# Performance work log

Hardware: AMD Instinct MI355X
Metric: run time of the kernel (lower is better)

## Reference

```python
import jax, jax.numpy as jnp
import numpy as np

H, KVH, HD, HID = 16, 8, 128, 2048
GROUPS = H // KVH
THETA = 10000.0
EPS = 1e-6


def _rms_norm(x, w):
    # x: (..., HD), norm in fp32 like Qwen3RMSNorm
    xf = x.astype(jnp.float32)
    var = jnp.mean(xf * xf, axis=-1, keepdims=True)
    return (xf * jax.lax.rsqrt(var + EPS)).astype(x.dtype) * w


def _rope_cos_sin(position_ids, dtype):
    # position_ids: (B, S) int
    inv_freq = 1.0 / (THETA ** (jnp.arange(0, HD, 2, dtype=jnp.float32) / HD))  # (HD/2,)
    freqs = position_ids.astype(jnp.float32)[..., None] * inv_freq  # (B, S, HD/2)
    emb = jnp.concatenate([freqs, freqs], axis=-1)  # (B, S, HD)
    return jnp.cos(emb).astype(dtype), jnp.sin(emb).astype(dtype)


def _rotate_half(x):
    x1, x2 = jnp.split(x, 2, axis=-1)
    return jnp.concatenate([-x2, x1], axis=-1)


def _apply_rope(q, k, cos, sin):
    # q,k: (B, h, S, HD); cos,sin: (B, S, HD) -> broadcast over head dim
    cos = cos[:, None, :, :]
    sin = sin[:, None, :, :]
    q = q * cos + _rotate_half(q) * sin
    k = k * cos + _rotate_half(k) * sin
    return q, k


def setup_inputs() -> dict:
    key = jax.random.key(0)
    ks = jax.random.split(key, 10)
    B, S, L = 1, 2048, 2048
    w = 0.02
    return {
        "hidden_states": jax.random.normal(ks[0], (B, S, HID), jnp.float32),
        "context": jax.random.normal(ks[1], (B, L, HID), jnp.float32),
        "position_ids": jnp.arange(S, dtype=jnp.int64)[None, :].repeat(B, axis=0),
        "Wq": jax.random.normal(ks[2], (H * HD, HID), jnp.float32) * w,
        "Wk": jax.random.normal(ks[3], (KVH * HD, HID), jnp.float32) * w,
        "Wv": jax.random.normal(ks[4], (KVH * HD, HID), jnp.float32) * w,
        "Wo": jax.random.normal(ks[5], (HID, H * HD), jnp.float32) * w,
        "Wk_ctx": jax.random.normal(ks[6], (KVH * HD, HID), jnp.float32) * w,
        "Wv_ctx": jax.random.normal(ks[7], (KVH * HD, HID), jnp.float32) * w,
        "q_norm_w": jnp.ones((HD,), jnp.float32),
        "k_norm_w": jnp.ones((HD,), jnp.float32),
    }


def reference(hidden_states, context, position_ids, Wq, Wk, Wv, Wo, Wk_ctx, Wv_ctx, q_norm_w, k_norm_w):
    B, S, _ = hidden_states.shape
    L = context.shape[1]
    scaling = HD ** -0.5

    Q = (hidden_states @ Wq.T).reshape(B, S, H, HD).transpose(0, 2, 1, 3)    # (B,H,S,HD)
    K = (hidden_states @ Wk.T).reshape(B, S, KVH, HD).transpose(0, 2, 1, 3)  # (B,KVH,S,HD)
    V = (hidden_states @ Wv.T).reshape(B, S, KVH, HD).transpose(0, 2, 1, 3)

    Q = _rms_norm(Q, q_norm_w)
    K = _rms_norm(K, k_norm_w)

    cos, sin = _rope_cos_sin(position_ids, Q.dtype)
    Q, K = _apply_rope(Q, K, cos, sin)

    K_ctx = (context @ Wk_ctx.T).reshape(B, L, KVH, HD).transpose(0, 2, 1, 3)
    V_ctx = (context @ Wv_ctx.T).reshape(B, L, KVH, HD).transpose(0, 2, 1, 3)

    K_full = jnp.concatenate([K_ctx, K], axis=2)  # (B,KVH,L+S,HD)
    V_full = jnp.concatenate([V_ctx, V], axis=2)
    K_full = jnp.repeat(K_full, GROUPS, axis=1)   # (B,H,L+S,HD)
    V_full = jnp.repeat(V_full, GROUPS, axis=1)

    attn = jnp.einsum("bhsd,bhtd->bhst", Q, K_full) * scaling  # (B,H,S,L+S)
    attn = jax.nn.softmax(attn.astype(jnp.float32), axis=-1).astype(Q.dtype)
    out = jnp.einsum("bhst,bhtd->bhsd", attn, V_full)          # (B,H,S,HD)
    out = out.transpose(0, 2, 1, 3).reshape(B, S, H * HD)
    return out @ Wo.T
```

## Files before the change

kernel.cpp:

```cpp
#include <hip/hip_runtime.h>

typedef __bf16 bf16_t;
typedef __attribute__((ext_vector_type(8))) __bf16 bf16x8;
typedef __attribute__((ext_vector_type(4))) __bf16 bf16x4;
typedef __attribute__((ext_vector_type(4))) float f32x4;

#define LDA_PAD 72

__device__ __forceinline__ bf16x8 ld8(const float* g) {
  f32x4 a = *(const f32x4*)g;
  f32x4 b = *(const f32x4*)(g + 4);
  bf16x8 r;
  r[0] = (bf16_t)a[0]; r[1] = (bf16_t)a[1]; r[2] = (bf16_t)a[2]; r[3] = (bf16_t)a[3];
  r[4] = (bf16_t)b[0]; r[5] = (bf16_t)b[1]; r[6] = (bf16_t)b[2]; r[7] = (bf16_t)b[3];
  return r;
}
__device__ __forceinline__ bf16x8 ld8(const bf16_t* g) { return *(const bf16x8*)g; }

struct CvtArgs { const float* src[8]; bf16_t* dst[8]; };

__global__ __launch_bounds__(256) void cvt_all(CvtArgs a) {
  const int g = blockIdx.x * 256 + threadIdx.x;
  int seg, base;
  if (g < 1048576)      { if (g < 524288)  { seg = 0; base = 0; }
                          else             { seg = 1; base = 524288; } }
  else if (g < 2097152) { if (g < 1572864) { seg = 2; base = 1048576; }
                          else if (g < 1835008) { seg = 3; base = 1572864; }
                          else             { seg = 4; base = 1835008; } }
  else                  { if (g < 2359296) { seg = 5; base = 2097152; }
                          else if (g < 2621440) { seg = 6; base = 2359296; }
                          else             { seg = 7; base = 2621440; } }
  const size_t off = (size_t)(g - base) * 8;
  *(bf16x8*)(a.dst[seg] + off) = ld8(a.src[seg] + off);
}

template<typename TI>
__global__ __launch_bounds__(256) void proj_all(
    const TI* __restrict__ hs, const TI* __restrict__ ctx,
    const TI* __restrict__ Wq, const TI* __restrict__ Wk,
    const TI* __restrict__ Wv, const TI* __restrict__ Wkc,
    const TI* __restrict__ Wvc,
    bf16_t* __restrict__ Qb, bf16_t* __restrict__ Kb, bf16_t* __restrict__ Vt)
{
  __shared__ __align__(16) bf16_t lA[128 * LDA_PAD];
  __shared__ __align__(16) bf16_t lB[128 * LDA_PAD];
  const int tid = threadIdx.x, wave = tid >> 6, lane = tid & 63;
  const int quad = lane >> 4, lc = lane & 15;
  const int u = blockIdx.x;
  const int xcd = u & 7, v = u >> 3;
  const int op = v >> 5, w = v & 31;
  const int nh = w >> 4, mt0 = w & 15;
  const int n0 = (xcd + nh * 8) * 128, m0 = mt0 * 128;
  const TI* A; const TI* B;
  if (op == 0) { A = hs; B = Wq + (size_t)n0 * 2048; }
  else {
    A = (op == 1) ? ctx : hs;
    const TI* WK = (op == 1) ? Wkc : Wk;
    const TI* WV = (op == 1) ? Wvc : Wv;
    B = (n0 < 1024) ? WK + (size_t)n0 * 2048 : WV + (size_t)(n0 - 1024) * 2048;
  }
  const int mw = (wave >> 1) * 64, nw = (wave & 1) * 64;
  const int lr8 = lane >> 3, lc8 = (lane & 7) * 8;

  f32x4 acc[4][4];
#pragma unroll
  for (int i = 0; i < 4; ++i)
#pragma unroll
    for (int j = 0; j < 4; ++j) acc[i][j] = (f32x4){0.f, 0.f, 0.f, 0.f};

  bf16x8 pa[4], pb[4];
#pragma unroll
  for (int i = 0; i < 4; ++i) {
    const int row = (wave + 4 * i) * 8 + lr8;
    pa[i] = ld8(A + (size_t)(m0 + row) * 2048 + lc8);
    pb[i] = ld8(B + (size_t)row * 2048 + lc8);
  }

  for (int k0 = 0; k0 < 2048; k0 += 64) {
    __syncthreads();
#pragma unroll
    for (int i = 0; i < 4; ++i) {
      const int row = (wave + 4 * i) * 8 + lr8;
      *(bf16x8*)(lA + row * LDA_PAD + lc8) = pa[i];
      *(bf16x8*)(lB + row * LDA_PAD + lc8) = pb[i];
    }
    __syncthreads();
    if (k0 + 64 < 2048) {
      const int kn = k0 + 64;
#pragma unroll
      for (int i = 0; i < 4; ++i) {
        const int row = (wave + 4 * i) * 8 + lr8;
        pa[i] = ld8(A + (size_t)(m0 + row) * 2048 + kn + lc8);
        pb[i] = ld8(B + (size_t)row * 2048 + kn + lc8);
      }
    }
#pragma unroll
    for (int kk = 0; kk < 2; ++kk) {
      bf16x8 af[4], bfv[4];
#pragma unroll
      for (int mt = 0; mt < 4; ++mt)
        af[mt] = *(const bf16x8*)(lA + (mw + mt * 16 + lc) * LDA_PAD + kk * 32 + quad * 8);
#pragma unroll
      for (int nt = 0; nt < 4; ++nt)
        bfv[nt] = *(const bf16x8*)(lB + (nw + nt * 16 + lc) * LDA_PAD + kk * 32 + quad * 8);
#pragma unroll
      for (int mt = 0; mt < 4; ++mt)
#pragma unroll
        for (int nt = 0; nt < 4; ++nt)
          acc[mt][nt] = __builtin_amdgcn_mfma_f32_16x16x32_bf16(af[mt], bfv[nt], acc[mt][nt], 0, 0, 0);
    }
  }

  if (op == 0) {
#pragma unroll
    for (int mt = 0; mt < 4; ++mt)
#pragma unroll
      for (int nt = 0; nt < 4; ++nt)
#pragma unroll
        for (int r = 0; r < 4; ++r)
          Qb[(size_t)(m0 + mw + mt * 16 + quad * 4 + r) * 2048 + n0 + nw + nt * 16 + lc]
              = (bf16_t)acc[mt][nt][r];
  } else {
    const int t_off = (op == 1) ? 0 : 2048;
    if (n0 < 1024) {
#pragma unroll
      for (int mt = 0; mt < 4; ++mt)
#pragma unroll
        for (int nt = 0; nt < 4; ++nt)
#pragma unroll
          for (int r = 0; r < 4; ++r) {
            const int n = n0 + nw + nt * 16 + lc;
            const int kvh = n >> 7, dd = n & 127;
            const int t = t_off + m0 + mw + mt * 16 + quad * 4 + r;
            Kb[((size_t)kvh * 4096 + t) * 128 + dd] = (bf16_t)acc[mt][nt][r];
          }
    } else {
#pragma unroll
      for (int mt = 0; mt < 4; ++mt)
#pragma unroll
        for (int nt = 0; nt < 4; ++nt) {
          const int n = n0 - 1024 + nw + nt * 16 + lc;
          const int kvh = n >> 7, dd = n & 127;
          const int t = t_off + m0 + mw + mt * 16 + quad * 4;
          bf16x4 pk;
#pragma unroll
          for (int r = 0; r < 4; ++r) pk[r] = (bf16_t)acc[mt][nt][r];
          *(bf16x4*)(Vt + ((size_t)kvh * 128 + dd) * 4096 + t) = pk;
        }
    }
  }
}

__global__ __launch_bounds__(256) void normrope(
    bf16_t* __restrict__ Q, bf16_t* __restrict__ Kb,
    const float* __restrict__ qw, const float* __restrict__ kw)
{
  const int wave = threadIdx.x >> 6, lane = threadIdx.x & 63;
  const int row = blockIdx.x * 4 + wave;
  bf16_t* p; const float* w; int pos;
  if (row < 32768) {
    const int s = row >> 4, hh = row & 15;
    p = Q + (size_t)s * 2048 + hh * 128; w = qw; pos = s;
  } else {
    const int rk = row - 32768;
    const int s = rk >> 3, hh = rk & 7;
    p = Kb + ((size_t)hh * 4096 + 2048 + s) * 128; w = kw; pos = s;
  }
  const float x1 = (float)p[lane], x2 = (float)p[lane + 64];
  float ss = x1 * x1 + x2 * x2;
#pragma unroll
  for (int m = 1; m < 64; m <<= 1) ss += __shfl_xor(ss, m, 64);
  const float inv = rsqrtf(ss * (1.0f / 128.0f) + 1e-6f);
  const float y1 = x1 * inv * w[lane];
  const float y2 = x2 * inv * w[lane + 64];
  const float freq = (float)pos * exp2f((float)lane * (-13.287712379549449f / 64.0f));
  const float cb = cosf(freq), sb = sinf(freq);
  p[lane]      = (bf16_t)(y1 * cb - y2 * sb);
  p[lane + 64] = (bf16_t)(y2 * cb + y1 * sb);
}

template<int SPLIT>
__global__ __launch_bounds__(512, 4) void attn_kernel(
    const bf16_t* __restrict__ Q, const bf16_t* __restrict__ Kb,
    const bf16_t* __restrict__ Vt, bf16_t* __restrict__ O,
    float* __restrict__ Of, float* __restrict__ Lf)
{
  __shared__ __align__(16) char lK[64 * 256];
  __shared__ __align__(16) char lV[128 * 128];
  __shared__ __align__(16) char lP[8 * 2048];
  const int tid = threadIdx.x, wave = tid >> 6, lane = tid & 63;
  const int quad = lane >> 4, lc = lane & 15;
  const int bid = blockIdx.x;
  const int hk = bid & 7, qt = (bid >> 3) & 15, hsel = (bid >> 7) & 1;
  const int half = SPLIT ? (bid >> 8) : 0;
  const int h = hk * 2 + hsel;
  const int mrow0 = qt * 128 + wave * 16;
  const int tbase = half * 2048;
  const int tend = tbase + (SPLIT ? 2048 : 4096);
  const float cexp = 0.08838834764831845f * 1.4426950408889634f;

  bf16x8 qf[4];
  {
    const bf16_t* qb = Q + (size_t)(mrow0 + lc) * 2048 + h * 128 + quad * 8;
#pragma unroll
    for (int ks = 0; ks < 4; ++ks) qf[ks] = *(const bf16x8*)(qb + ks * 32);
  }
  float rs[4] = {0.f, 0.f, 0.f, 0.f};
  f32x4 oacc[8];
#pragma unroll
  for (int ot = 0; ot < 8; ++ot) oacc[ot] = (f32x4){0.f, 0.f, 0.f, 0.f};

  bf16x8 kp[2], vp[2];
  auto load_tile = [&](int t0) {
    const bf16_t* Kt = Kb + ((size_t)hk * 4096 + t0) * 128;
    const bf16_t* Vb = Vt + (size_t)hk * 524288 + t0;
#pragma unroll
    for (int i = 0; i < 2; ++i) {
      const int idx = wave * 2 + i;
      kp[i] = *(const bf16x8*)(Kt + (size_t)(idx * 4 + quad) * 128 + lc * 8);
      vp[i] = *(const bf16x8*)(Vb + (size_t)(idx * 8 + (lane >> 3)) * 4096 + (lane & 7) * 8);
    }
  };
  load_tile(tbase);

  char* lPw = lP + wave * 2048;
  const int sw_rd = (lc & 7) << 4;

  for (int t0 = tbase; t0 < tend; t0 += 64) {
    __syncthreads();
#pragma unroll
    for (int i = 0; i < 2; ++i) {
      const int idx = wave * 2 + i;
      const int kr = idx * 4 + quad;
      *(bf16x8*)(lK + kr * 256 + ((lc * 16) ^ ((kr & 7) << 4))) = kp[i];
      const int vr = idx * 8 + (lane >> 3);
      *(bf16x8*)(lV + vr * 128 + (((lane & 7) * 16) ^ ((vr & 7) << 4))) = vp[i];
    }
    __syncthreads();
    if (t0 + 64 < tend) load_tile(t0 + 64);

    f32x4 s[4];
#pragma unroll
    for (int nt = 0; nt < 4; ++nt) {
      f32x4 a = (f32x4){0.f, 0.f, 0.f, 0.f};
#pragma unroll
      for (int ks = 0; ks < 4; ++ks) {
        bf16x8 kf = *(const bf16x8*)(lK + (nt * 16 + lc) * 256 + ((ks * 64 + quad * 16) ^ sw_rd));
        a = __builtin_amdgcn_mfma_f32_16x16x32_bf16(qf[ks], kf, a, 0, 0, 0);
      }
      s[nt] = a;
    }

#pragma unroll
    for (int nt = 0; nt < 4; ++nt)
#pragma unroll
      for (int r = 0; r < 4; ++r) {
        const float pv = exp2f(s[nt][r] * cexp);
        rs[r] += pv;
        const int pr = quad * 4 + r;
        *(bf16_t*)(lPw + pr * 128 + ((nt * 32 + lc * 2) ^ ((pr & 7) << 4))) = (bf16_t)pv;
      }

#pragma unroll
    for (int ks2 = 0; ks2 < 2; ++ks2) {
      bf16x8 pf = *(const bf16x8*)(lPw + lc * 128 + ((ks2 * 64 + quad * 16) ^ sw_rd));
#pragma unroll
      for (int ot = 0; ot < 8; ++ot) {
        bf16x8 vf = *(const bf16x8*)(lV + (ot * 16 + lc) * 128 + ((ks2 * 64 + quad * 16) ^ sw_rd));
        oacc[ot] = __builtin_amdgcn_mfma_f32_16x16x32_bf16(pf, vf, oacc[ot], 0, 0, 0);
      }
    }
  }

  float l_r[4];
#pragma unroll
  for (int r = 0; r < 4; ++r) {
    float vv = rs[r];
    vv += __shfl_xor(vv, 1, 64);
    vv += __shfl_xor(vv, 2, 64);
    vv += __shfl_xor(vv, 4, 64);
    vv += __shfl_xor(vv, 8, 64);
    l_r[r] = vv;
  }
  if (SPLIT) {
    float* Oh = Of + (size_t)half * 4194304;
#pragma unroll
    for (int ot = 0; ot < 8; ++ot)
#pragma unroll
      for (int r = 0; r < 4; ++r)
        Oh[(size_t)(mrow0 + quad * 4 + r) * 2048 + h * 128 + ot * 16 + lc] = oacc[ot][r];
    if (lc == 0) {
      float* Lh = Lf + half * 32768 + h * 2048 + mrow0;
#pragma unroll
      for (int r = 0; r < 4; ++r) Lh[quad * 4 + r] = l_r[r];
    }
  } else {
#pragma unroll
    for (int ot = 0; ot < 8; ++ot)
#pragma unroll
      for (int r = 0; r < 4; ++r)
        O[(size_t)(mrow0 + quad * 4 + r) * 2048 + h * 128 + ot * 16 + lc]
            = (bf16_t)(oacc[ot][r] / l_r[r]);
  }
}

__global__ __launch_bounds__(256) void combine(
    const float* __restrict__ Of, const float* __restrict__ Lf,
    bf16_t* __restrict__ Ob)
{
  const int b = blockIdx.x;
  const int hk = b & 7, idx = b >> 3;
  const int h = hk * 2 + (idx & 1), sg = idx >> 1;
  const int t = threadIdx.x;
  const int s = sg * 16 + (t >> 4), d = (t & 15) * 8;
  const size_t e = (size_t)s * 2048 + h * 128 + d;
  const float l = Lf[h * 2048 + s] + Lf[32768 + h * 2048 + s];
  const float inv = 1.0f / l;
  f32x4 a0 = *(const f32x4*)(Of + e);
  f32x4 a1 = *(const f32x4*)(Of + e + 4);
  f32x4 b0 = *(const f32x4*)(Of + 4194304 + e);
  f32x4 b1 = *(const f32x4*)(Of + 4194304 + e + 4);
  bf16x8 rr;
#pragma unroll
  for (int j = 0; j < 4; ++j) {
    rr[j]     = (bf16_t)((a0[j] + b0[j]) * inv);
    rr[4 + j] = (bf16_t)((a1[j] + b1[j]) * inv);
  }
  *(bf16x8*)(Ob + e) = rr;
}

template<typename TB>
__global__ __launch_bounds__(256) void gemm_o(
    const bf16_t* __restrict__ A, const TB* __restrict__ Bw,
    float* __restrict__ C)
{
  __shared__ __align__(16) bf16_t lA[128 * LDA_PAD];
  __shared__ __align__(16) bf16_t lB[64 * LDA_PAD];
  const int tid = threadIdx.x, wave = tid >> 6, lane = tid & 63;
  const int quad = lane >> 4, lc = lane & 15;
  const int bid = blockIdx.x;
  const int xcd = bid & 7, v = bid >> 3;
  const int nh = v >> 4, mt0 = v & 15;
  const int n0 = (xcd + nh * 8) * 64, m0 = mt0 * 128;
  const int mw = (wave >> 1) * 64, nw = (wave & 1) * 32;
  const int lr8 = lane >> 3, lc8 = (lane & 7) * 8;

  f32x4 acc[4][2];
#pragma unroll
  for (int i = 0; i < 4; ++i)
#pragma unroll
    for (int j = 0; j < 2; ++j) acc[i][j] = (f32x4){0.f, 0.f, 0.f, 0.f};

  bf16x8 pa[4], pb[2];
#pragma unroll
  for (int i = 0; i < 4; ++i)
    pa[i] = ld8(A + (size_t)(m0 + (wave + 4 * i) * 8 + lr8) * 2048 + lc8);
#pragma unroll
  for (int i = 0; i < 2; ++i)
    pb[i] = ld8(Bw + (size_t)(n0 + i * 32 + wave * 8 + lr8) * 2048 + lc8);

  for (int k0 = 0; k0 < 2048; k0 += 64) {
    __syncthreads();
#pragma unroll
    for (int i = 0; i < 4; ++i)
      *(bf16x8*)(lA + ((wave + 4 * i) * 8 + lr8) * LDA_PAD + lc8) = pa[i];
#pragma unroll
    for (int i = 0; i < 2; ++i)
      *(bf16x8*)(lB + (i * 32 + wave * 8 + lr8) * LDA_PAD + lc8) = pb[i];
    __syncthreads();
    if (k0 + 64 < 2048) {
      const int kn = k0 + 64;
#pragma unroll
      for (int i = 0; i < 4; ++i)
        pa[i] = ld8(A + (size_t)(m0 + (wave + 4 * i) * 8 + lr8) * 2048 + kn + lc8);
#pragma unroll
      for (int i = 0; i < 2; ++i)
        pb[i] = ld8(Bw + (size_t)(n0 + i * 32 + wave * 8 + lr8) * 2048 + kn + lc8);
    }
#pragma unroll
    for (int kk = 0; kk < 2; ++kk) {
      bf16x8 af[4], bfv[2];
#pragma unroll
      for (int mt = 0; mt < 4; ++mt)
        af[mt] = *(const bf16x8*)(lA + (mw + mt * 16 + lc) * LDA_PAD + kk * 32 + quad * 8);
#pragma unroll
      for (int nt = 0; nt < 2; ++nt)
        bfv[nt] = *(const bf16x8*)(lB + (nw + nt * 16 + lc) * LDA_PAD + kk * 32 + quad * 8);
#pragma unroll
      for (int mt = 0; mt < 4; ++mt)
#pragma unroll
        for (int nt = 0; nt < 2; ++nt)
          acc[mt][nt] = __builtin_amdgcn_mfma_f32_16x16x32_bf16(af[mt], bfv[nt], acc[mt][nt], 0, 0, 0);
    }
  }
#pragma unroll
  for (int mt = 0; mt < 4; ++mt)
#pragma unroll
    for (int nt = 0; nt < 2; ++nt)
#pragma unroll
      for (int r = 0; r < 4; ++r)
        C[(size_t)(m0 + mw + mt * 16 + quad * 4 + r) * 2048 + n0 + nw + nt * 16 + lc]
            = acc[mt][nt][r];
}

extern "C" void kernel_launch(void* const* d_in, const int* in_sizes, int n_in,
                              void* d_out, int out_size, void* d_ws, size_t ws_size,
                              hipStream_t stream)
{
  const float* hs  = (const float*)d_in[0];
  const float* ctx = (const float*)d_in[1];
  const float* Wq  = (const float*)d_in[3];
  const float* Wk  = (const float*)d_in[4];
  const float* Wv  = (const float*)d_in[5];
  const float* Wo  = (const float*)d_in[6];
  const float* Wkc = (const float*)d_in[7];
  const float* Wvc = (const float*)d_in[8];
  const float* qw  = (const float*)d_in[9];
  const float* kw  = (const float*)d_in[10];

  bf16_t* Kb = (bf16_t*)d_out;
  bf16_t* Vt = Kb + (size_t)4 * 1024 * 1024;
  bf16_t* wsb = (bf16_t*)d_ws;
  const bool fast = ws_size >= (size_t)64 * 1024 * 1024;

  dim3 blk(256), ablk(512);
  if (fast) {
    bf16_t* hs_b  = wsb;
    bf16_t* ctx_b = wsb + (size_t)8  * 524288;
    bf16_t* Wq_b  = wsb + (size_t)16 * 524288;
    bf16_t* Wk_b  = wsb + (size_t)24 * 524288;
    bf16_t* Wv_b  = wsb + (size_t)28 * 524288;
    bf16_t* Wkc_b = wsb + (size_t)32 * 524288;
    bf16_t* Wvc_b = wsb + (size_t)36 * 524288;
    bf16_t* Wo_b  = wsb + (size_t)40 * 524288;
    bf16_t* Qb    = wsb + (size_t)48 * 524288;
    bf16_t* Ob    = wsb + (size_t)56 * 524288;
    float*  Of    = (float*)wsb;
    float*  Lfp   = (float*)(wsb + (size_t)16 * 1024 * 1024);
    CvtArgs ca;
    ca.src[0] = hs;  ca.dst[0] = hs_b;
    ca.src[1] = ctx; ca.dst[1] = ctx_b;
    ca.src[2] = Wq;  ca.dst[2] = Wq_b;
    ca.src[3] = Wk;  ca.dst[3] = Wk_b;
    ca.src[4] = Wv;  ca.dst[4] = Wv_b;
    ca.src[5] = Wkc; ca.dst[5] = Wkc_b;
    ca.src[6] = Wvc; ca.dst[6] = Wvc_b;
    ca.src[7] = Wo;  ca.dst[7] = Wo_b;
    cvt_all<<<dim3(12288), blk, 0, stream>>>(ca);
    proj_all<bf16_t><<<dim3(768), blk, 0, stream>>>(
        hs_b, ctx_b, Wq_b, Wk_b, Wv_b, Wkc_b, Wvc_b, Qb, Kb, Vt);
    normrope<<<dim3(12288), blk, 0, stream>>>(Qb, Kb, qw, kw);
    attn_kernel<1><<<dim3(512), ablk, 0, stream>>>(Qb, Kb, Vt, nullptr, Of, Lfp);
    combine<<<dim3(2048), blk, 0, stream>>>(Of, Lfp, Ob);
    gemm_o<bf16_t><<<dim3(512), blk, 0, stream>>>(Ob, Wo_b, (float*)d_out);
  } else {
    bf16_t* Qb = wsb;
    bf16_t* Ob = wsb + (size_t)8 * 524288;
    proj_all<float><<<dim3(768), blk, 0, stream>>>(
        hs, ctx, Wq, Wk, Wv, Wkc, Wvc, Qb, Kb, Vt);
    normrope<<<dim3(12288), blk, 0, stream>>>(Qb, Kb, qw, kw);
    attn_kernel<0><<<dim3(256), ablk, 0, stream>>>(Qb, Kb, Vt, Ob, nullptr, nullptr);
    gemm_o<float><<<dim3(512), blk, 0, stream>>>(Ob, Wo, (float*)d_out);
  }
}
```

Before: 350.2 us.

## Fuse RMSNorm and RoPE into projection GEMM epilogue, drop normrope kernel

Moves the per-head RMSNorm and rotary embedding for Q and the self K into the epilogue of the projection GEMM. Row sums of squares are reduced across the two column-waves through shared memory, and the rotate-half partner values are exchanged through a float staging buffer. This removes a separate kernel launch plus a full read and write of Q and K. In exchange it adds several block barriers and per-element cos/sin work inside the GEMM epilogue, which lengthens those blocks and could create load imbalance against the V and context-K blocks.

New measurement: 542.8 us. +55.0%, slower.

```diff
diff --git a/kernel.cpp b/kernel.cpp
--- a/kernel.cpp
+++ b/kernel.cpp
@@ -34,16 +34,18 @@
   *(bf16x8*)(a.dst[seg] + off) = ld8(a.src[seg] + off);
 }
 
-template<typename TI>
+template<typename TA>
 __global__ __launch_bounds__(256) void proj_all(
-    const TI* __restrict__ hs, const TI* __restrict__ ctx,
-    const TI* __restrict__ Wq, const TI* __restrict__ Wk,
-    const TI* __restrict__ Wv, const TI* __restrict__ Wkc,
-    const TI* __restrict__ Wvc,
+    const TA* __restrict__ hs, const TA* __restrict__ ctx,
+    const TA* __restrict__ Wq, const TA* __restrict__ Wk,
+    const TA* __restrict__ Wv, const TA* __restrict__ Wkc,
+    const TA* __restrict__ Wvc,
+    const float* __restrict__ qw, const float* __restrict__ kw,
     bf16_t* __restrict__ Qb, bf16_t* __restrict__ Kb, bf16_t* __restrict__ Vt)
 {
-  __shared__ __align__(16) bf16_t lA[128 * LDA_PAD];
-  __shared__ __align__(16) bf16_t lB[128 * LDA_PAD];
+  __shared__ __align__(16) char smem[2 * 128 * LDA_PAD * 2];
+  bf16_t* lA = (bf16_t*)smem;
+  bf16_t* lB = lA + 128 * LDA_PAD;
   const int tid = threadIdx.x, wave = tid >> 6, lane = tid & 63;
   const int quad = lane >> 4, lc = lane & 15;
   const int u = blockIdx.x;
@@ -51,12 +53,12 @@
   const int op = v >> 5, w = v & 31;
   const int nh = w >> 4, mt0 = w & 15;
   const int n0 = (xcd + nh * 8) * 128, m0 = mt0 * 128;
-  const TI* A; const TI* B;
+  const TA* A; const TA* B;
   if (op == 0) { A = hs; B = Wq + (size_t)n0 * 2048; }
   else {
     A = (op == 1) ? ctx : hs;
-    const TI* WK = (op == 1) ? Wkc : Wk;
-    const TI* WV = (op == 1) ? Wvc : Wv;
+    const TA* WK = (op == 1) ? Wkc : Wk;
+    const TA* WV = (op == 1) ? Wvc : Wv;
     B = (n0 < 1024) ? WK + (size_t)n0 * 2048 : WV + (size_t)(n0 - 1024) * 2048;
   }
   const int mw = (wave >> 1) * 64, nw = (wave & 1) * 64;
@@ -111,72 +113,113 @@
     }
   }
 
-  if (op == 0) {
+  const bool normQ = (op == 0);
+  const bool normK = (op == 2) && (n0 < 1024);
+  if (normQ || normK) {
+    const float* wgt = normQ ? qw : kw;
+    float wf[4];
+#pragma unroll
+    for (int nt = 0; nt < 4; ++nt) wf[nt] = wgt[nw + nt * 16 + lc];
+
+    float ss[4][4];
 #pragma unroll
     for (int mt = 0; mt < 4; ++mt)
 #pragma unroll
+      for (int r = 0; r < 4; ++r) {
+        float s = 0.f;
+#pragma unroll
+        for (int nt = 0; nt < 4; ++nt) s += acc[mt][nt][r] * acc[mt][nt][r];
+#pragma unroll
+        for (int m = 1; m < 16; m <<= 1) s += __shfl_xor(s, m, 16);
+        ss[mt][r] = s;
+      }
+    __syncthreads();
+    float* ssbuf = (float*)(smem + 32768);
+    if (lc == 0) {
+#pragma unroll
+      for (int mt = 0; mt < 4; ++mt)
+#pragma unroll
+        for (int r = 0; r < 4; ++r)
+          ssbuf[((wave >> 1) * 64 + mt * 16 + quad * 4 + r) * 2 + (wave & 1)] = ss[mt][r];
+    }
+    __syncthreads();
+    float inv[4][4];
+#pragma unroll
+    for (int mt = 0; mt < 4; ++mt)
+#pragma unroll
+      for (int r = 0; r < 4; ++r) {
+        const int row = (wave >> 1) * 64 + mt * 16 + quad * 4 + r;
+        const float t = ssbuf[row * 2] + ssbuf[row * 2 + 1];
+        inv[mt][r] = rsqrtf(t * (1.0f / 128.0f) + 1e-6f);
+      }
+
+    float invf[4];
+#pragma unroll
+    for (int nt = 0; nt < 4; ++nt)
+      invf[nt] = exp2f((float)(nt * 16 + lc) * (-13.287712379549449f / 64.0f));
+
+    float* ybuf = (float*)smem;
+    const int kvh = n0 >> 7;
+#pragma unroll
+    for (int mt = 0; mt < 4; ++mt) {
+      __syncthreads();
+#pragma unroll
       for (int nt = 0; nt < 4; ++nt)
 #pragma unroll
-        for (int r = 0; r < 4; ++r)
-          Qb[(size_t)(m0 + mw + mt * 16 + quad * 4 + r) * 2048 + n0 + nw + nt * 16 + lc]
-              = (bf16_t)acc[mt][nt][r];
+        for (int r = 0; r < 4; ++r) {
+          const int yrow = (wave >> 1) * 16 + quad * 4 + r;
+          ybuf[yrow * 132 + nw + nt * 16 + lc] = acc[mt][nt][r] * inv[mt][r] * wf[nt];
+        }
+      __syncthreads();
+#pragma unroll
+      for (int nt = 0; nt < 4; ++nt)
+#pragma unroll
+        for (int r = 0; r < 4; ++r) {
+          const int yrow = (wave >> 1) * 16 + quad * 4 + r;
+          const int col = nw + nt * 16 + lc;
+          const int row = (wave >> 1) * 64 + mt * 16 + quad * 4 + r;
+          const float yv = acc[mt][nt][r] * inv[mt][r] * wf[nt];
+          const float y2 = ybuf[yrow * 132 + (col ^ 64)];
+          const int pos = m0 + row;
+          const float fr = (float)pos * invf[nt];
+          const float cb = cosf(fr), sb = sinf(fr);
+          const float out = (nw == 0) ? (yv * cb - y2 * sb) : (yv * cb + y2 * sb);
+          if (normQ) {
+            Qb[(size_t)(m0 + row) * 2048 + n0 + col] = (bf16_t)out;
+          } else {
+            const int t = 2048 + m0 + row;
+            Kb[((size_t)kvh * 4096 + t) * 128 + col] = (bf16_t)out;
+          }
+        }
+    }
+  } else if (n0 < 1024) {
+    const int t_off = 0;
+#pragma unroll
+    for (int mt = 0; mt < 4; ++mt)
+#pragma unroll
+      for (int nt = 0; nt < 4; ++nt)
+#pragma unroll
+        for (int r = 0; r < 4; ++r) {
+          const int n = n0 + nw + nt * 16 + lc;
+          const int kvh = n >> 7, dd = n & 127;
+          const int t = t_off + m0 + mw + mt * 16 + quad * 4 + r;
+          Kb[((size_t)kvh * 4096 + t) * 128 + dd] = (bf16_t)acc[mt][nt][r];
+        }
   } else {
     const int t_off = (op == 1) ? 0 : 2048;
-    if (n0 < 1024) {
-#pragma unroll
-      for (int mt = 0; mt < 4; ++mt)
-#pragma unroll
-        for (int nt = 0; nt < 4; ++nt)
-#pragma unroll
-          for (int r = 0; r < 4; ++r) {
-            const int n = n0 + nw + nt * 16 + lc;
-            const int kvh = n >> 7, dd = n & 127;
-            const int t = t_off + m0 + mw + mt * 16 + quad * 4 + r;
-            Kb[((size_t)kvh * 4096 + t) * 128 + dd] = (bf16_t)acc[mt][nt][r];
-          }
-    } else {
-#pragma unroll
-      for (int mt = 0; mt < 4; ++mt)
-#pragma unroll
-        for (int nt = 0; nt < 4; ++nt) {
-          const int n = n0 - 1024 + nw + nt * 16 + lc;
-          const int kvh = n >> 7, dd = n & 127;
-          const int t = t_off + m0 + mw + mt * 16 + quad * 4;
-          bf16x4 pk;
-#pragma unroll
-          for (int r = 0; r < 4; ++r) pk[r] = (bf16_t)acc[mt][nt][r];
-          *(bf16x4*)(Vt + ((size_t)kvh * 128 + dd) * 4096 + t) = pk;
-        }
-    }
-  }
-}
-
-__global__ __launch_bounds__(256) void normrope(
-    bf16_t* __restrict__ Q, bf16_t* __restrict__ Kb,
-    const float* __restrict__ qw, const float* __restrict__ kw)
-{
-  const int wave = threadIdx.x >> 6, lane = threadIdx.x & 63;
-  const int row = blockIdx.x * 4 + wave;
-  bf16_t* p; const float* w; int pos;
-  if (row < 32768) {
-    const int s = row >> 4, hh = row & 15;
-    p = Q + (size_t)s * 2048 + hh * 128; w = qw; pos = s;
-  } else {
-    const int rk = row - 32768;
-    const int s = rk >> 3, hh = rk & 7;
-    p = Kb + ((size_t)hh * 4096 + 2048 + s) * 128; w = kw; pos = s;
-  }
-  const float x1 = (float)p[lane], x2 = (float)p[lane + 64];
-  float ss = x1 * x1 + x2 * x2;
-#pragma unroll
-  for (int m = 1; m < 64; m <<= 1) ss += __shfl_xor(ss, m, 64);
-  const float inv = rsqrtf(ss * (1.0f / 128.0f) + 1e-6f);
-  const float y1 = x1 * inv * w[lane];
-  const float y2 = x2 * inv * w[lane + 64];
-  const float freq = (float)pos * exp2f((float)lane * (-13.287712379549449f / 64.0f));
-  const float cb = cosf(freq), sb = sinf(freq);
-  p[lane]      = (bf16_t)(y1 * cb - y2 * sb);
-  p[lane + 64] = (bf16_t)(y2 * cb + y1 * sb);
+#pragma unroll
+    for (int mt = 0; mt < 4; ++mt)
+#pragma unroll
+      for (int nt = 0; nt < 4; ++nt) {
+        const int n = n0 - 1024 + nw + nt * 16 + lc;
+        const int kvh = n >> 7, dd = n & 127;
+        const int t = t_off + m0 + mw + mt * 16 + quad * 4;
+        bf16x4 pk;
+#pragma unroll
+        for (int r = 0; r < 4; ++r) pk[r] = (bf16_t)acc[mt][nt][r];
+        *(bf16x4*)(Vt + ((size_t)kvh * 128 + dd) * 4096 + t) = pk;
+      }
+  }
 }
 
 template<int SPLIT>
@@ -448,8 +491,7 @@
     ca.src[7] = Wo;  ca.dst[7] = Wo_b;
     cvt_all<<<dim3(12288), blk, 0, stream>>>(ca);
     proj_all<bf16_t><<<dim3(768), blk, 0, stream>>>(
-        hs_b, ctx_b, Wq_b, Wk_b, Wv_b, Wkc_b, Wvc_b, Qb, Kb, Vt);
-    normrope<<<dim3(12288), blk, 0, stream>>>(Qb, Kb, qw, kw);
+        hs_b, ctx_b, Wq_b, Wk_b, Wv_b, Wkc_b, Wvc_b, qw, kw, Qb, Kb, Vt);
     attn_kernel<1><<<dim3(512), ablk, 0, stream>>>(Qb, Kb, Vt, nullptr, Of, Lfp);
     combine<<<dim3(2048), blk, 0, stream>>>(Of, Lfp, Ob);
     gemm_o<bf16_t><<<dim3(512), blk, 0, stream>>>(Ob, Wo_b, (float*)d_out);
@@ -457,8 +499,7 @@
     bf16_t* Qb = wsb;
     bf16_t* Ob = wsb + (size_t)8 * 524288;
     proj_all<float><<<dim3(768), blk, 0, stream>>>(
-        hs, ctx, Wq, Wk, Wv, Wkc, Wvc, Qb, Kb, Vt);
-    normrope<<<dim3(12288), blk, 0, stream>>>(Qb, Kb, qw, kw);
+        hs, ctx, Wq, Wk, Wv, Wkc, Wvc, qw, kw, Qb, Kb, Vt);
     attn_kernel<0><<<dim3(256), ablk, 0, stream>>>(Qb, Kb, Vt, Ob, nullptr, nullptr);
     gemm_o<float><<<dim3(512), blk, 0, stream>>>(Ob, Wo, (float*)d_out);
   }
```

## Fuse QK norm+RoPE into projection epilogue and combine into attention via grid barrier

Applied to the files above, without the earlier changes.

Drops the separate normrope kernel: the projection GEMM now stages each 128x128 Q/K tile in shared memory and applies RMSNorm and RoPE before writing. It also drops the separate combine launch: after writing split partials, attention blocks sync through an atomic counter grid barrier and then merge the two halves themselves. This saves two launches and a round trip of Q/K through global memory. The cost is recomputing cos/sin per element and a spin-wait barrier that only works if all 512 blocks are resident at once.

New measurement: 530.6 us. +51.5%, slower.

```diff
diff --git a/kernel.cpp b/kernel.cpp
--- a/kernel.cpp
+++ b/kernel.cpp
@@ -40,13 +40,17 @@
     const TI* __restrict__ Wq, const TI* __restrict__ Wk,
     const TI* __restrict__ Wv, const TI* __restrict__ Wkc,
     const TI* __restrict__ Wvc,
-    bf16_t* __restrict__ Qb, bf16_t* __restrict__ Kb, bf16_t* __restrict__ Vt)
+    const float* __restrict__ qw, const float* __restrict__ kw,
+    bf16_t* __restrict__ Qb, bf16_t* __restrict__ Kb, bf16_t* __restrict__ Vt,
+    unsigned int* __restrict__ ctr)
 {
-  __shared__ __align__(16) bf16_t lA[128 * LDA_PAD];
-  __shared__ __align__(16) bf16_t lB[128 * LDA_PAD];
+  __shared__ __align__(16) char smem[2 * 128 * LDA_PAD * 2];
+  bf16_t* lA = (bf16_t*)smem;
+  bf16_t* lB = lA + 128 * LDA_PAD;
   const int tid = threadIdx.x, wave = tid >> 6, lane = tid & 63;
   const int quad = lane >> 4, lc = lane & 15;
   const int u = blockIdx.x;
+  if (ctr && u == 0 && tid == 0) *ctr = 0;
   const int xcd = u & 7, v = u >> 3;
   const int op = v >> 5, w = v & 31;
   const int nh = w >> 4, mt0 = w & 15;
@@ -111,79 +115,88 @@
     }
   }
 
-  if (op == 0) {
+  const bool normQ = (op == 0);
+  const bool normK = (op == 2) && (n0 < 1024);
+  if (normQ || normK) {
+    bf16_t* yb = (bf16_t*)smem;
+    __syncthreads();
 #pragma unroll
     for (int mt = 0; mt < 4; ++mt)
 #pragma unroll
       for (int nt = 0; nt < 4; ++nt)
 #pragma unroll
         for (int r = 0; r < 4; ++r)
-          Qb[(size_t)(m0 + mw + mt * 16 + quad * 4 + r) * 2048 + n0 + nw + nt * 16 + lc]
+          yb[(mw + mt * 16 + quad * 4 + r) * 136 + nw + nt * 16 + lc]
               = (bf16_t)acc[mt][nt][r];
+    __syncthreads();
+    const int rowi = tid >> 1, half = tid & 1;
+    const float* wgt = normQ ? qw : kw;
+    const bf16_t* rowp = yb + rowi * 136;
+    float ss = 0.f;
+#pragma unroll
+    for (int c = 0; c < 8; ++c) {
+      bf16x8 vv = *(const bf16x8*)(rowp + half * 64 + c * 8);
+#pragma unroll
+      for (int j = 0; j < 8; ++j) { const float f = (float)vv[j]; ss += f * f; }
+    }
+    ss += __shfl_xor(ss, 1, 64);
+    const float inv = rsqrtf(ss * (1.0f / 128.0f) + 1e-6f);
+    const int pos = m0 + rowi;
+    const int kvh = n0 >> 7;
+    bf16_t* dst = normQ ? (Qb + (size_t)pos * 2048 + n0 + half * 64)
+                        : (Kb + ((size_t)kvh * 4096 + 2048 + m0 + rowi) * 128 + half * 64);
+    const float sgn = half ? 1.f : -1.f;
+#pragma unroll
+    for (int c = 0; c < 8; ++c) {
+      bf16x8 vv = *(const bf16x8*)(rowp + half * 64 + c * 8);
+      bf16x8 v2 = *(const bf16x8*)(rowp + (half ^ 1) * 64 + c * 8);
+      bf16x8 o;
+#pragma unroll
+      for (int j = 0; j < 8; ++j) {
+        const int dd = half * 64 + c * 8 + j;
+        const int dm = c * 8 + j;
+        const float y  = (float)vv[j] * inv * wgt[dd];
+        const float y2 = (float)v2[j] * inv * wgt[dd ^ 64];
+        const float fr = (float)pos * exp2f((float)dm * (-13.287712379549449f / 64.0f));
+        o[j] = (bf16_t)(y * cosf(fr) + sgn * y2 * sinf(fr));
+      }
+      *(bf16x8*)dst = o; dst += 8;
+    }
+  } else if (n0 < 1024) {
+#pragma unroll
+    for (int mt = 0; mt < 4; ++mt)
+#pragma unroll
+      for (int nt = 0; nt < 4; ++nt)
+#pragma unroll
+        for (int r = 0; r < 4; ++r) {
+          const int n = n0 + nw + nt * 16 + lc;
+          const int kvh = n >> 7, dd = n & 127;
+          const int t = m0 + mw + mt * 16 + quad * 4 + r;
+          Kb[((size_t)kvh * 4096 + t) * 128 + dd] = (bf16_t)acc[mt][nt][r];
+        }
   } else {
     const int t_off = (op == 1) ? 0 : 2048;
-    if (n0 < 1024) {
-#pragma unroll
-      for (int mt = 0; mt < 4; ++mt)
-#pragma unroll
-        for (int nt = 0; nt < 4; ++nt)
-#pragma unroll
-          for (int r = 0; r < 4; ++r) {
-            const int n = n0 + nw + nt * 16 + lc;
-            const int kvh = n >> 7, dd = n & 127;
-            const int t = t_off + m0 + mw + mt * 16 + quad * 4 + r;
-            Kb[((size_t)kvh * 4096 + t) * 128 + dd] = (bf16_t)acc[mt][nt][r];
-          }
-    } else {
-#pragma unroll
-      for (int mt = 0; mt < 4; ++mt)
-#pragma unroll
-        for (int nt = 0; nt < 4; ++nt) {
-          const int n = n0 - 1024 + nw + nt * 16 + lc;
-          const int kvh = n >> 7, dd = n & 127;
-          const int t = t_off + m0 + mw + mt * 16 + quad * 4;
-          bf16x4 pk;
-#pragma unroll
-          for (int r = 0; r < 4; ++r) pk[r] = (bf16_t)acc[mt][nt][r];
-          *(bf16x4*)(Vt + ((size_t)kvh * 128 + dd) * 4096 + t) = pk;
-        }
-    }
-  }
-}
-
-__global__ __launch_bounds__(256) void normrope(
-    bf16_t* __restrict__ Q, bf16_t* __restrict__ Kb,
-    const float* __restrict__ qw, const float* __restrict__ kw)
-{
-  const int wave = threadIdx.x >> 6, lane = threadIdx.x & 63;
-  const int row = blockIdx.x * 4 + wave;
-  bf16_t* p; const float* w; int pos;
-  if (row < 32768) {
-    const int s = row >> 4, hh = row & 15;
-    p = Q + (size_t)s * 2048 + hh * 128; w = qw; pos = s;
-  } else {
-    const int rk = row - 32768;
-    const int s = rk >> 3, hh = rk & 7;
-    p = Kb + ((size_t)hh * 4096 + 2048 + s) * 128; w = kw; pos = s;
-  }
-  const float x1 = (float)p[lane], x2 = (float)p[lane + 64];
-  float ss = x1 * x1 + x2 * x2;
-#pragma unroll
-  for (int m = 1; m < 64; m <<= 1) ss += __shfl_xor(ss, m, 64);
-  const float inv = rsqrtf(ss * (1.0f / 128.0f) + 1e-6f);
-  const float y1 = x1 * inv * w[lane];
-  const float y2 = x2 * inv * w[lane + 64];
-  const float freq = (float)pos * exp2f((float)lane * (-13.287712379549449f / 64.0f));
-  const float cb = cosf(freq), sb = sinf(freq);
-  p[lane]      = (bf16_t)(y1 * cb - y2 * sb);
-  p[lane + 64] = (bf16_t)(y2 * cb + y1 * sb);
+#pragma unroll
+    for (int mt = 0; mt < 4; ++mt)
+#pragma unroll
+      for (int nt = 0; nt < 4; ++nt) {
+        const int n = n0 - 1024 + nw + nt * 16 + lc;
+        const int kvh = n >> 7, dd = n & 127;
+        const int t = t_off + m0 + mw + mt * 16 + quad * 4;
+        bf16x4 pk;
+#pragma unroll
+        for (int r = 0; r < 4; ++r) pk[r] = (bf16_t)acc[mt][nt][r];
+        *(bf16x4*)(Vt + ((size_t)kvh * 128 + dd) * 4096 + t) = pk;
+      }
+  }
 }
 
 template<int SPLIT>
 __global__ __launch_bounds__(512, 4) void attn_kernel(
     const bf16_t* __restrict__ Q, const bf16_t* __restrict__ Kb,
     const bf16_t* __restrict__ Vt, bf16_t* __restrict__ O,
-    float* __restrict__ Of, float* __restrict__ Lf)
+    float* __restrict__ Of, float* __restrict__ Lf,
+    bf16_t* __restrict__ Ob, unsigned int* __restrict__ ctr)
 {
   __shared__ __align__(16) char lK[64 * 256];
   __shared__ __align__(16) char lV[128 * 128];
@@ -294,6 +307,34 @@
 #pragma unroll
       for (int r = 0; r < 4; ++r) Lh[quad * 4 + r] = l_r[r];
     }
+    __threadfence();
+    __syncthreads();
+    if (tid == 0) {
+      atomicAdd(ctr, 1u);
+      while (atomicAdd(ctr, 0u) < gridDim.x) __builtin_amdgcn_s_sleep(8);
+      __threadfence();
+    }
+    __syncthreads();
+#pragma unroll
+    for (int it = 0; it < 2; ++it) {
+      const int g = bid * 512 + tid + it * 262144;
+      const size_t e = (size_t)g * 8;
+      const int s = (int)(e >> 11);
+      const int hh = ((int)(e & 2047)) >> 7;
+      const float l = Lf[hh * 2048 + s] + Lf[32768 + hh * 2048 + s];
+      const float invl = 1.0f / l;
+      f32x4 a0 = *(const f32x4*)(Of + e);
+      f32x4 a1 = *(const f32x4*)(Of + e + 4);
+      f32x4 b0 = *(const f32x4*)(Of + 4194304 + e);
+      f32x4 b1 = *(const f32x4*)(Of + 4194304 + e + 4);
+      bf16x8 rr;
+#pragma unroll
+      for (int j = 0; j < 4; ++j) {
+        rr[j]     = (bf16_t)((a0[j] + b0[j]) * invl);
+        rr[4 + j] = (bf16_t)((a1[j] + b1[j]) * invl);
+      }
+      *(bf16x8*)(Ob + e) = rr;
+    }
   } else {
 #pragma unroll
     for (int ot = 0; ot < 8; ++ot)
@@ -302,31 +343,6 @@
         O[(size_t)(mrow0 + quad * 4 + r) * 2048 + h * 128 + ot * 16 + lc]
             = (bf16_t)(oacc[ot][r] / l_r[r]);
   }
-}
-
-__global__ __launch_bounds__(256) void combine(
-    const float* __restrict__ Of, const float* __restrict__ Lf,
-    bf16_t* __restrict__ Ob)
-{
-  const int b = blockIdx.x;
-  const int hk = b & 7, idx = b >> 3;
-  const int h = hk * 2 + (idx & 1), sg = idx >> 1;
-  const int t = threadIdx.x;
-  const int s = sg * 16 + (t >> 4), d = (t & 15) * 8;
-  const size_t e = (size_t)s * 2048 + h * 128 + d;
-  const float l = Lf[h * 2048 + s] + Lf[32768 + h * 2048 + s];
-  const float inv = 1.0f / l;
-  f32x4 a0 = *(const f32x4*)(Of + e);
-  f32x4 a1 = *(const f32x4*)(Of + e + 4);
-  f32x4 b0 = *(const f32x4*)(Of + 4194304 + e);
-  f32x4 b1 = *(const f32x4*)(Of + 4194304 + e + 4);
-  bf16x8 rr;
-#pragma unroll
-  for (int j = 0; j < 4; ++j) {
-    rr[j]     = (bf16_t)((a0[j] + b0[j]) * inv);
-    rr[4 + j] = (bf16_t)((a1[j] + b1[j]) * inv);
-  }
-  *(bf16x8*)(Ob + e) = rr;
 }
 
 template<typename TB>
@@ -403,6 +419,29 @@
             = acc[mt][nt][r];
 }
 
+__global__ __launch_bounds__(256) void combine(
+    const float* __restrict__ Of, const float* __restrict__ Lf,
+    bf16_t* __restrict__ Ob)
+{
+  const int g = blockIdx.x * 256 + threadIdx.x;
+  const size_t e = (size_t)g * 8;
+  const int s = (int)(e >> 11);
+  const int hh = ((int)(e & 2047)) >> 7;
+  const float l = Lf[hh * 2048 + s] + Lf[32768 + hh * 2048 + s];
+  const float invl = 1.0f / l;
+  f32x4 a0 = *(const f32x4*)(Of + e);
+  f32x4 a1 = *(const f32x4*)(Of + e + 4);
+  f32x4 b0 = *(const f32x4*)(Of + 4194304 + e);
+  f32x4 b1 = *(const f32x4*)(Of + 4194304 + e + 4);
+  bf16x8 rr;
+#pragma unroll
+  for (int j = 0; j < 4; ++j) {
+    rr[j]     = (bf16_t)((a0[j] + b0[j]) * invl);
+    rr[4 + j] = (bf16_t)((a1[j] + b1[j]) * invl);
+  }
+  *(bf16x8*)(Ob + e) = rr;
+}
+
 extern "C" void kernel_launch(void* const* d_in, const int* in_sizes, int n_in,
                               void* d_out, int out_size, void* d_ws, size_t ws_size,
                               hipStream_t stream)
@@ -436,7 +475,8 @@
     bf16_t* Qb    = wsb + (size_t)48 * 524288;
     bf16_t* Ob    = wsb + (size_t)56 * 524288;
     float*  Of    = (float*)wsb;
-    float*  Lfp   = (float*)(wsb + (size_t)16 * 1024 * 1024);
+    float*  Lfp   = (float*)((char*)d_ws + (size_t)32 * 1024 * 1024);
+    unsigned int* ctr = (unsigned int*)((char*)d_ws + (size_t)33 * 1024 * 1024);
     CvtArgs ca;
     ca.src[0] = hs;  ca.dst[0] = hs_b;
     ca.src[1] = ctx; ca.dst[1] = ctx_b;
@@ -448,18 +488,17 @@
     ca.src[7] = Wo;  ca.dst[7] = Wo_b;
     cvt_all<<<dim3(12288), blk, 0, stream>>>(ca);
     proj_all<bf16_t><<<dim3(768), blk, 0, stream>>>(
-        hs_b, ctx_b, Wq_b, Wk_b, Wv_b, Wkc_b, Wvc_b, Qb, Kb, Vt);
-    normrope<<<dim3(12288), blk, 0, stream>>>(Qb, Kb, qw, kw);
-    attn_kernel<1><<<dim3(512), ablk, 0, stream>>>(Qb, Kb, Vt, nullptr, Of, Lfp);
-    combine<<<dim3(2048), blk, 0, stream>>>(Of, Lfp, Ob);
+        hs_b, ctx_b, Wq_b, Wk_b, Wv_b, Wkc_b, Wvc_b, qw, kw, Qb, Kb, Vt, ctr);
+    attn_kernel<1><<<dim3(512), ablk, 0, stream>>>(
+        Qb, Kb, Vt, nullptr, Of, Lfp, Ob, ctr);
     gemm_o<bf16_t><<<dim3(512), blk, 0, stream>>>(Ob, Wo_b, (float*)d_out);
   } else {
     bf16_t* Qb = wsb;
     bf16_t* Ob = wsb + (size_t)8 * 524288;
     proj_all<float><<<dim3(768), blk, 0, stream>>>(
-        hs, ctx, Wq, Wk, Wv, Wkc, Wvc, Qb, Kb, Vt);
-    normrope<<<dim3(12288), blk, 0, stream>>>(Qb, Kb, qw, kw);
-    attn_kernel<0><<<dim3(256), ablk, 0, stream>>>(Qb, Kb, Vt, Ob, nullptr, nullptr);
+        hs, ctx, Wq, Wk, Wv, Wkc, Wvc, qw, kw, Qb, Kb, Vt, nullptr);
+    attn_kernel<0><<<dim3(256), ablk, 0, stream>>>(
+        Qb, Kb, Vt, Ob, nullptr, nullptr, nullptr, nullptr);
     gemm_o<float><<<dim3(512), blk, 0, stream>>>(Ob, Wo, (float*)d_out);
   }
 }
```
